# Kernel optimization log

Hardware: AMD Instinct MI355X
Metric: run time of the kernel (lower is better)

## Reference

```python
import jax, jax.numpy as jnp
import numpy as np

N_NODES = 50000
N_EDGES = 800000
NEG_SLOPE = 0.2


def gat_conv(x, src, dst, W, att_src, att_dst, bias, heads, out_ch, concat):
    """PyG-style GATConv (eval mode, self-loops already included in src/dst)."""
    N = x.shape[0]
    h = (x @ W).reshape(N, heads, out_ch)                      # [N,H,C]
    a_src = (h * att_src).sum(-1)                              # [N,H]
    a_dst = (h * att_dst).sum(-1)                              # [N,H]
    alpha = jax.nn.leaky_relu(a_src[src] + a_dst[dst], NEG_SLOPE)  # [E,H]
    # numerically stable segment softmax over incoming edges of each dst node
    amax = jax.ops.segment_max(alpha, dst, num_segments=N)     # [N,H]
    amax = jax.lax.stop_gradient(jnp.where(jnp.isfinite(amax), amax, 0.0))
    ex = jnp.exp(alpha - amax[dst])                            # [E,H]
    denom = jax.ops.segment_sum(ex, dst, num_segments=N)       # [N,H]
    coef = ex / (denom[dst] + 1e-16)                           # [E,H]
    msg = h[src] * coef[..., None]                             # [E,H,C]
    out = jax.ops.segment_sum(msg, dst, num_segments=N)        # [N,H,C]
    out = out.reshape(N, heads * out_ch) if concat else out.mean(axis=1)
    return out + bias


def setup_inputs() -> dict:
    key = jax.random.key(0)
    ks = jax.random.split(key, 12)
    x = jax.random.normal(ks[0], (N_NODES, 2), dtype=jnp.float32)
    edge_index = jax.random.randint(ks[1], (2, N_EDGES), 0, N_NODES, dtype=jnp.int64)
    # layer1: 2 -> 32, heads=4, concat
    W1 = jax.random.normal(ks[2], (2, 4 * 32), dtype=jnp.float32) * 0.5
    att_src1 = jax.random.normal(ks[3], (1, 4, 32), dtype=jnp.float32) * 0.1
    att_dst1 = jax.random.normal(ks[4], (1, 4, 32), dtype=jnp.float32) * 0.1
    b1 = jax.random.normal(ks[5], (128,), dtype=jnp.float32) * 0.01
    # layer2: 128 -> 128, heads=1, concat=False
    W2 = jax.random.normal(ks[6], (128, 128), dtype=jnp.float32) * (1.0 / np.sqrt(128.0))
    att_src2 = jax.random.normal(ks[7], (1, 1, 128), dtype=jnp.float32) * 0.1
    att_dst2 = jax.random.normal(ks[8], (1, 1, 128), dtype=jnp.float32) * 0.1
    b2 = jax.random.normal(ks[9], (128,), dtype=jnp.float32) * 0.01
    return {"x": x, "edge_index": edge_index, "W1": W1, "att_src1": att_src1,
            "att_dst1": att_dst1, "b1": b1, "W2": W2, "att_src2": att_src2,
            "att_dst2": att_dst2, "b2": b2}


def reference(x, edge_index, W1, att_src1, att_dst1, b1, W2, att_src2, att_dst2, b2):
    N = x.shape[0]
    loops = jnp.arange(N, dtype=edge_index.dtype)
    src = jnp.concatenate([edge_index[0], loops])  # PyG add_self_loops=True
    dst = jnp.concatenate([edge_index[1], loops])
    h = gat_conv(x, src, dst, W1, att_src1, att_dst1, b1, 4, 32, True)
    h = jax.nn.relu(h)
    h = gat_conv(h, src, dst, W2, att_src2, att_dst2, b2, 1, 128, False)
    # global_mean_pool with a single graph (batch all zeros) then squeeze(0)
    return h.mean(axis=0)  # [128]
```

## Files before the change

kernel.cpp:

```cpp
#include <hip/hip_runtime.h>

#define NN 50000
#define NE 800000
#define ET (NE + NN)
#define EPW 4096
#define NWGP ((ET + EPW - 1) / EPW)
#define NB 196
#define BCAP 6144

typedef unsigned short u16;
typedef unsigned int u32;
typedef unsigned char u8;

__device__ __forceinline__ float lrelu(float a) { return a > 0.f ? a : 0.2f * a; }

__global__ __launch_bounds__(256) void k_init(
        u32* __restrict__ bcur, u32* __restrict__ bcur2,
        u32* __restrict__ ovf, u32* __restrict__ ovf2,
        float* __restrict__ z, int* __restrict__ off, int* __restrict__ off_s,
        const float* __restrict__ W1, const float* __restrict__ as1,
        const float* __restrict__ ad1, const float* __restrict__ W2,
        const float* __restrict__ as2, const float* __restrict__ ad2,
        float* __restrict__ AD, float* __restrict__ vs, float* __restrict__ vd) {
    int i = threadIdx.x;
    bcur[i] = 0; bcur2[i] = 0;
    if (i == 0) { *ovf = 0; *ovf2 = 0; off[NN] = ET; off_s[NN] = ET; }
    if (i < 128) {
        z[i] = 0.f;
        float a = 0.f, d = 0.f;
        for (int c = 0; c < 128; ++c) {
            float wv = W2[i * 128 + c];
            a = fmaf(wv, as2[c], a);
            d = fmaf(wv, ad2[c], d);
        }
        vs[i] = a; vd[i] = d;
    }
    if (i >= 128 && i < 144) {
        int q = i - 128, isD = q >> 3, j = (q >> 2) & 1, hd = q & 3;
        const float* att = isD ? ad1 : as1;
        float acc = 0.f;
        for (int ch = 0; ch < 32; ++ch)
            acc = fmaf(W1[j * 128 + hd * 32 + ch], att[hd * 32 + ch], acc);
        AD[isD * 8 + j * 4 + hd] = acc;
    }
}

__global__ __launch_bounds__(256) void k_part(
        const int* __restrict__ ei,
        u32* __restrict__ bcur, u32* __restrict__ bcur2,
        u32* __restrict__ stg, u32* __restrict__ stg_s,
        u32* __restrict__ stg2, u32* __restrict__ stg2s,
        u32* __restrict__ ovf, u32* __restrict__ ovf2) {
    __shared__ u32 lcnt[256], sc[256], lbase[256], gbase[256];
    __shared__ u32 lpair[EPW];
    __shared__ u8  lbkt[EPW];
    int t = threadIdx.x;
    int e0 = blockIdx.x * EPW;

    u32 pr[16]; bool vd_[16]; u16 rk[16]; u8 bk[16];
#pragma unroll
    for (int j = 0; j < 16; ++j) {
        int e = e0 + j * 256 + t;
        vd_[j] = (e < ET);
        if (vd_[j]) {
            int s, d;
            if (e < NE) { s = ei[e]; d = ei[NE + e]; } else { s = d = e - NE; }
            pr[j] = ((u32)d << 16) | (u32)s;
        }
    }
    lcnt[t] = 0;
    __syncthreads();
#pragma unroll
    for (int j = 0; j < 16; ++j) if (vd_[j]) {
        int b = pr[j] >> 24;
        bk[j] = (u8)b;
        rk[j] = (u16)atomicAdd(&lcnt[b], 1u);
    }
    __syncthreads();
    u32 v = lcnt[t];
    sc[t] = v;
    __syncthreads();
#pragma unroll
    for (int st = 1; st < 256; st <<= 1) {
        u32 u = (t >= st) ? sc[t - st] : 0;
        __syncthreads();
        sc[t] += u;
        __syncthreads();
    }
    lbase[t] = sc[t] - v;
    gbase[t] = atomicAdd(&bcur[t], v);
    __syncthreads();
#pragma unroll
    for (int j = 0; j < 16; ++j) if (vd_[j]) {
        u32 idx = lbase[bk[j]] + rk[j];
        lpair[idx] = pr[j];
        lbkt[idx]  = bk[j];
    }
    __syncthreads();
    int nloc = lbase[255] + lcnt[255];
    for (int i = t; i < nloc; i += 256) {
        u32 b = lbkt[i];
        u32 g = gbase[b] + (i - lbase[b]);
        u32 p = lpair[i];
        if (g < BCAP) stg[(size_t)b * BCAP + g] = p;
        else { u32 o = atomicAdd(ovf, 1u); if (o < 4096) stg2[o] = p; }
    }
    __syncthreads();
    lcnt[t] = 0;
    __syncthreads();
#pragma unroll
    for (int j = 0; j < 16; ++j) if (vd_[j]) {
        int b = (pr[j] & 0xFFFFu) >> 8;
        bk[j] = (u8)b;
        rk[j] = (u16)atomicAdd(&lcnt[b], 1u);
    }
    __syncthreads();
    v = lcnt[t];
    sc[t] = v;
    __syncthreads();
#pragma unroll
    for (int st = 1; st < 256; st <<= 1) {
        u32 u = (t >= st) ? sc[t - st] : 0;
        __syncthreads();
        sc[t] += u;
        __syncthreads();
    }
    lbase[t] = sc[t] - v;
    gbase[t] = atomicAdd(&bcur2[t], v);
    __syncthreads();
#pragma unroll
    for (int j = 0; j < 16; ++j) if (vd_[j]) {
        u32 p2 = (pr[j] << 16) | (pr[j] >> 16);
        u32 idx = lbase[bk[j]] + rk[j];
        lpair[idx] = p2;
        lbkt[idx]  = bk[j];
    }
    __syncthreads();
    nloc = lbase[255] + lcnt[255];
    for (int i = t; i < nloc; i += 256) {
        u32 b = lbkt[i];
        u32 g = gbase[b] + (i - lbase[b]);
        u32 p = lpair[i];
        if (g < BCAP) stg_s[(size_t)b * BCAP + g] = p;
        else { u32 o = atomicAdd(ovf2, 1u); if (o < 4096) stg2s[o] = p; }
    }
}

__global__ __launch_bounds__(256) void k_place2(
        const u32* __restrict__ bcurA, const u32* __restrict__ bcurB,
        const u32* __restrict__ stgA, const u32* __restrict__ stgB,
        const u32* __restrict__ stg2A, const u32* __restrict__ stg2B,
        const u32* __restrict__ ovfA, const u32* __restrict__ ovfB,
        int* __restrict__ offA, int* __restrict__ offB,
        u16* __restrict__ outA, u16* __restrict__ outB) {
    __shared__ u32 sh[256], hist[256], sc[256], lcur[256];
    __shared__ u16 lcsr[BCAP];
    int blk = blockIdx.x, t = threadIdx.x;
    bool isB = (blk >= NB);
    int b = isB ? blk - NB : blk;
    const u32* bcur = isB ? bcurB : bcurA;
    const u32* stg  = isB ? stgB  : stgA;
    const u32* stg2 = isB ? stg2B : stg2A;
    const u32* ovf  = isB ? ovfB  : ovfA;
    int* off   = isB ? offB : offA;
    u16* out16 = isB ? outB : outA;

    u32 vv = (t < NB) ? bcur[t] : 0;
    sh[t] = vv;
    hist[t] = 0;
    __syncthreads();
#pragma unroll
    for (int s = 1; s < 256; s <<= 1) {
        u32 u = (t >= s) ? sh[t - s] : 0;
        __syncthreads();
        sh[t] += u;
        __syncthreads();
    }
    int S0 = (int)(sh[b] - bcur[b]);
    u32 cnt = bcur[b];
    u32 cmain = min(cnt, (u32)BCAP);

    for (u32 i = t; i < cmain; i += 256)
        atomicAdd(&hist[(stg[(size_t)b * BCAP + i] >> 16) & 255u], 1u);
    if (cnt > cmain) {
        u32 no = min(*ovf, 4096u);
        for (u32 i = t; i < no; i += 256) {
            u32 p = stg2[i];
            if ((p >> 24) == (u32)b) atomicAdd(&hist[(p >> 16) & 255u], 1u);
        }
    }
    __syncthreads();
    u32 v = hist[t];
    sc[t] = v;
    __syncthreads();
#pragma unroll
    for (int s = 1; s < 256; s <<= 1) {
        u32 u = (t >= s) ? sc[t - s] : 0;
        __syncthreads();
        sc[t] += u;
        __syncthreads();
    }
    u32 lexcl = sc[t] - v;
    int n = (b << 8) + t;
    if (n < NN) off[n] = S0 + (int)lexcl;
    lcur[t] = lexcl;
    __syncthreads();
    bool direct = (cnt > (u32)BCAP);
    for (u32 i = t; i < cmain; i += 256) {
        u32 p = stg[(size_t)b * BCAP + i];
        u32 r = atomicAdd(&lcur[(p >> 16) & 255u], 1u);
        if (direct) out16[S0 + r] = (u16)(p & 0xFFFFu);
        else        lcsr[r] = (u16)(p & 0xFFFFu);
    }
    if (cnt > cmain) {
        u32 no = min(*ovf, 4096u);
        for (u32 i = t; i < no; i += 256) {
            u32 p = stg2[i];
            if ((p >> 24) == (u32)b) {
                u32 r = atomicAdd(&lcur[(p >> 16) & 255u], 1u);
                if (direct) out16[S0 + r] = (u16)(p & 0xFFFFu);
                else        lcsr[r] = (u16)(p & 0xFFFFu);
            }
        }
    }
    __syncthreads();
    if (!direct)
        for (u32 i = t; i < cnt; i += 256) out16[S0 + i] = lcsr[i];
}

__global__ __launch_bounds__(128) void k_agg1x(
        const int* __restrict__ off, const u16* __restrict__ csr,
        const float* __restrict__ x, const float* __restrict__ AD,
        const float* __restrict__ W1, const float* __restrict__ b1,
        const float* __restrict__ vs, const float* __restrict__ vd,
        float* __restrict__ x2, float* __restrict__ asrc2,
        float* __restrict__ adst2) {
    __shared__ float sW1[256], sb1[128], svs[128], svd[128];
    int t = threadIdx.x;
    if (t < 128) {
        sW1[t] = W1[t]; sW1[128 + t] = W1[128 + t];
        sb1[t] = b1[t]; svs[t] = vs[t]; svd[t] = vd[t];
    }
    __syncthreads();
    int g = t >> 4, li = t & 15;
    int n = blockIdx.x * 8 + g;
    if (n >= NN) return;
    int e0 = off[n], deg = off[n + 1] - e0;
    float2 xd = *(const float2*)(x + 2 * n);
    float A0[4], A1[4], adn[4];
#pragma unroll
    for (int h = 0; h < 4; ++h) {
        A0[h] = AD[h]; A1[h] = AD[4 + h];
        adn[h] = fmaf(AD[8 + h], xd.x, AD[12 + h] * xd.y);
    }

    float den[4] = {0.f, 0.f, 0.f, 0.f};
    float S0[4] = {0.f, 0.f, 0.f, 0.f};
    float S1[4] = {0.f, 0.f, 0.f, 0.f};
    for (int e = li; e < deg; e += 16) {
        int s = csr[e0 + e];
        float2 xv = *(const float2*)(x + 2 * s);
#pragma unroll
        for (int h = 0; h < 4; ++h) {
            float al = lrelu(fmaf(A0[h], xv.x, A1[h] * xv.y) + adn[h]);
            float ex = __expf(fminf(al, 80.f));
            den[h] += ex;
            S0[h] = fmaf(ex, xv.x, S0[h]);
            S1[h] = fmaf(ex, xv.y, S1[h]);
        }
    }
#pragma unroll
    for (int m = 8; m >= 1; m >>= 1) {
#pragma unroll
        for (int h = 0; h < 4; ++h) {
            den[h] += __shfl_xor(den[h], m);
            S0[h]  += __shfl_xor(S0[h], m);
            S1[h]  += __shfl_xor(S1[h], m);
        }
    }
    float inv[4];
#pragma unroll
    for (int h = 0; h < 4; ++h) inv[h] = 1.f / (den[h] + 1e-16f);

    int hd = li >> 2;
    float ov[8];
    float ps = 0.f, pd = 0.f;
#pragma unroll
    for (int k = 0; k < 8; ++k) {
        int c = li * 8 + k;
        float o = (S0[hd] * sW1[c] + S1[hd] * sW1[128 + c]) * inv[hd];
        float v = fmaxf(o + sb1[c], 0.f);
        ov[k] = v;
        ps = fmaf(v, svs[c], ps);
        pd = fmaf(v, svd[c], pd);
    }
    *(float4*)(x2 + (size_t)n * 128 + li * 8) =
        make_float4(ov[0], ov[1], ov[2], ov[3]);
    *(float4*)(x2 + (size_t)n * 128 + li * 8 + 4) =
        make_float4(ov[4], ov[5], ov[6], ov[7]);
#pragma unroll
    for (int m = 8; m >= 1; m >>= 1) {
        ps += __shfl_xor(ps, m);
        pd += __shfl_xor(pd, m);
    }
    if (li == 0) { asrc2[n] = ps; adst2[n] = pd; }
}

__global__ __launch_bounds__(128) void k_den(
        const int* __restrict__ off, const u16* __restrict__ csr,
        const float* __restrict__ asrc2, const float* __restrict__ adst2,
        float2* __restrict__ dd) {
    int t = threadIdx.x;
    int g = t >> 4, li = t & 15;
    int n = blockIdx.x * 8 + g;
    if (n >= NN) return;
    int e0 = off[n], deg = off[n + 1] - e0;
    float adn = adst2[n];
    float den = 0.f;
    for (int e = li; e < deg; e += 16)
        den += __expf(fminf(lrelu(asrc2[csr[e0 + e]] + adn), 80.f));
#pragma unroll
    for (int m = 8; m >= 1; m >>= 1) den += __shfl_xor(den, m);
    if (li == 0) dd[n] = make_float2(adn, 1.f / (den + 1e-16f));
}

__global__ __launch_bounds__(128) void k_wgath(
        const int* __restrict__ off_s, const u16* __restrict__ csc,
        const float* __restrict__ asrc2, const float2* __restrict__ dd,
        float* __restrict__ w) {
    int t = threadIdx.x;
    int g = t >> 4, li = t & 15;
    int n = blockIdx.x * 8 + g;
    if (n >= NN) return;
    int e0 = off_s[n], deg = off_s[n + 1] - e0;
    float as = asrc2[n];
    float acc = 0.f;
    for (int e = li; e < deg; e += 16) {
        float2 di = dd[csc[e0 + e]];
        acc = fmaf(__expf(fminf(lrelu(as + di.x), 80.f)), di.y, acc);
    }
#pragma unroll
    for (int m = 8; m >= 1; m >>= 1) acc += __shfl_xor(acc, m);
    if (li == 0) w[n] = acc;
}

__global__ __launch_bounds__(256) void k_wsum(const float* __restrict__ w,
                                              const float* __restrict__ x2,
                                              float* __restrict__ z) {
    __shared__ float red[256];
    int t = threadIdx.x, c = t & 127, rp = t >> 7;
    float acc = 0.f;
    for (int n = blockIdx.x * 2 + rp; n < NN; n += 2048)
        acc = fmaf(w[n], x2[(size_t)n * 128 + c], acc);
    red[t] = acc;
    __syncthreads();
    if (t < 128) atomicAdd(z + t, red[t] + red[t + 128]);
}

__global__ __launch_bounds__(128) void k_out(const float* __restrict__ z,
                                             const float* __restrict__ W2,
                                             const float* __restrict__ b2,
                                             float* __restrict__ out) {
    int c = threadIdx.x;
    float acc = 0.f;
    for (int k = 0; k < 128; ++k)
        acc = fmaf(z[k], W2[k * 128 + c], acc);
    out[c] = b2[c] + acc * (1.0f / NN);
}

extern "C" void kernel_launch(void* const* d_in, const int* in_sizes, int n_in,
                              void* d_out, int out_size, void* d_ws, size_t ws_size,
                              hipStream_t stream) {
    const float* x   = (const float*)d_in[0];
    const int*   ei  = (const int*)d_in[1];
    const float* W1  = (const float*)d_in[2];
    const float* as1 = (const float*)d_in[3];
    const float* ad1 = (const float*)d_in[4];
    const float* b1  = (const float*)d_in[5];
    const float* W2  = (const float*)d_in[6];
    const float* as2 = (const float*)d_in[7];
    const float* ad2 = (const float*)d_in[8];
    const float* b2  = (const float*)d_in[9];
    float* out = (float*)d_out;

    char* ws     = (char*)d_ws;
    float* x2    = (float*)ws;
    u32*  stg    = (u32*)x2;
    u32*  stg_s  = stg + (size_t)NB * BCAP;
    float* w     = x2 + (size_t)NN * 128;
    float* asrc2 = w + NN;
    float* adst2 = asrc2 + NN;
    float2* dd   = (float2*)(adst2 + NN);
    int* off     = (int*)(dd + NN);
    int* off_s   = off + NN + 1;
    u32* bcur    = (u32*)(off_s + NN + 1);
    u32* bcur2   = bcur + 256;
    u32* ovf     = bcur2 + 256;
    u32* ovf2    = ovf + 4;
    u32* stg2    = ovf2 + 4;
    u32* stg2s   = stg2 + 4096;
    u16* csr16   = (u16*)(stg2s + 4096);
    u16* csc16   = csr16 + ET;
    float* AD    = (float*)(csc16 + ET);
    float* vs    = AD + 16;
    float* vd    = vs + 128;
    float* z     = vd + 128;

    k_init<<<1, 256, 0, stream>>>(bcur, bcur2, ovf, ovf2, z, off, off_s,
                                  W1, as1, ad1, W2, as2, ad2, AD, vs, vd);
    k_part<<<NWGP, 256, 0, stream>>>(ei, bcur, bcur2, stg, stg_s,
                                     stg2, stg2s, ovf, ovf2);
    k_place2<<<2 * NB, 256, 0, stream>>>(bcur, bcur2, stg, stg_s,
                                         stg2, stg2s, ovf, ovf2,
                                         off, off_s, csr16, csc16);
    k_agg1x<<<(NN + 7) / 8, 128, 0, stream>>>(off, csr16, x, AD, W1, b1,
                                              vs, vd, x2, asrc2, adst2);
    k_den<<<(NN + 7) / 8, 128, 0, stream>>>(off, csr16, asrc2, adst2, dd);
    k_wgath<<<(NN + 7) / 8, 128, 0, stream>>>(off_s, csc16, asrc2, dd, w);
    k_wsum<<<1024, 256, 0, stream>>>(w, x2, z);
    k_out<<<1, 128, 0, stream>>>(z, W2, b2, out);
}
```

Before: 123.5 us.

## Use wave-shuffle scans, halve partition tile, fuse final reduction with output

Replaces the shared-memory Hillis-Steele prefix scans (many __syncthreads per scan) with a 64-lane shuffle scan plus a 4-wave combine in the partition and placement kernels. Halves edges per partition workgroup so more workgroups run and fewer registers are needed per thread. Fuses the final weighted-sum and output matmul kernels using a last-block-done counter, removing one launch. The trade-offs are more global atomics on the bucket counters from the extra workgroups and a grid-wide completion counter that relies on correct fencing.

```diff
diff --git a/kernel.cpp b/kernel.cpp
--- a/kernel.cpp
+++ b/kernel.cpp
@@ -3,10 +3,12 @@
 #define NN 50000
 #define NE 800000
 #define ET (NE + NN)
-#define EPW 4096
+#define EPW 2048
+#define EPT (EPW / 256)
 #define NWGP ((ET + EPW - 1) / EPW)
 #define NB 196
 #define BCAP 6144
+#define WSB 1024
 
 typedef unsigned short u16;
 typedef unsigned int u32;
@@ -14,9 +16,18 @@
 
 __device__ __forceinline__ float lrelu(float a) { return a > 0.f ? a : 0.2f * a; }
 
+__device__ __forceinline__ u32 wave_iscan(u32 v, int lane) {
+#pragma unroll
+    for (int d = 1; d < 64; d <<= 1) {
+        u32 u = __shfl_up(v, d);
+        if (lane >= d) v += u;
+    }
+    return v;
+}
+
 __global__ __launch_bounds__(256) void k_init(
         u32* __restrict__ bcur, u32* __restrict__ bcur2,
-        u32* __restrict__ ovf, u32* __restrict__ ovf2,
+        u32* __restrict__ ovf, u32* __restrict__ ovf2, u32* __restrict__ cnt,
         float* __restrict__ z, int* __restrict__ off, int* __restrict__ off_s,
         const float* __restrict__ W1, const float* __restrict__ as1,
         const float* __restrict__ ad1, const float* __restrict__ W2,
@@ -24,7 +35,7 @@
         float* __restrict__ AD, float* __restrict__ vs, float* __restrict__ vd) {
     int i = threadIdx.x;
     bcur[i] = 0; bcur2[i] = 0;
-    if (i == 0) { *ovf = 0; *ovf2 = 0; off[NN] = ET; off_s[NN] = ET; }
+    if (i == 0) { *ovf = 0; *ovf2 = 0; *cnt = 0; off[NN] = ET; off_s[NN] = ET; }
     if (i < 128) {
         z[i] = 0.f;
         float a = 0.f, d = 0.f;
@@ -51,15 +62,16 @@
         u32* __restrict__ stg, u32* __restrict__ stg_s,
         u32* __restrict__ stg2, u32* __restrict__ stg2s,
         u32* __restrict__ ovf, u32* __restrict__ ovf2) {
-    __shared__ u32 lcnt[256], sc[256], lbase[256], gbase[256];
+    __shared__ u32 lcnt[256], lbase[256], gbase[256], wsums[4];
     __shared__ u32 lpair[EPW];
     __shared__ u8  lbkt[EPW];
     int t = threadIdx.x;
+    int lane = t & 63, wid = t >> 6;
     int e0 = blockIdx.x * EPW;
 
-    u32 pr[16]; bool vd_[16]; u16 rk[16]; u8 bk[16];
-#pragma unroll
-    for (int j = 0; j < 16; ++j) {
+    u32 pr[EPT]; bool vd_[EPT]; u16 rk[EPT]; u8 bk[EPT];
+#pragma unroll
+    for (int j = 0; j < EPT; ++j) {
         int e = e0 + j * 256 + t;
         vd_[j] = (e < ET);
         if (vd_[j]) {
@@ -71,27 +83,24 @@
     lcnt[t] = 0;
     __syncthreads();
 #pragma unroll
-    for (int j = 0; j < 16; ++j) if (vd_[j]) {
+    for (int j = 0; j < EPT; ++j) if (vd_[j]) {
         int b = pr[j] >> 24;
         bk[j] = (u8)b;
         rk[j] = (u16)atomicAdd(&lcnt[b], 1u);
     }
     __syncthreads();
     u32 v = lcnt[t];
-    sc[t] = v;
-    __syncthreads();
-#pragma unroll
-    for (int st = 1; st < 256; st <<= 1) {
-        u32 u = (t >= st) ? sc[t - st] : 0;
-        __syncthreads();
-        sc[t] += u;
-        __syncthreads();
-    }
-    lbase[t] = sc[t] - v;
+    u32 inc = wave_iscan(v, lane);
+    if (lane == 63) wsums[wid] = inc;
+    __syncthreads();
+    u32 base = 0;
+#pragma unroll
+    for (int k = 0; k < 4; ++k) base += (k < wid) ? wsums[k] : 0;
+    lbase[t] = base + inc - v;
     gbase[t] = atomicAdd(&bcur[t], v);
     __syncthreads();
 #pragma unroll
-    for (int j = 0; j < 16; ++j) if (vd_[j]) {
+    for (int j = 0; j < EPT; ++j) if (vd_[j]) {
         u32 idx = lbase[bk[j]] + rk[j];
         lpair[idx] = pr[j];
         lbkt[idx]  = bk[j];
@@ -109,27 +118,24 @@
     lcnt[t] = 0;
     __syncthreads();
 #pragma unroll
-    for (int j = 0; j < 16; ++j) if (vd_[j]) {
+    for (int j = 0; j < EPT; ++j) if (vd_[j]) {
         int b = (pr[j] & 0xFFFFu) >> 8;
         bk[j] = (u8)b;
         rk[j] = (u16)atomicAdd(&lcnt[b], 1u);
     }
     __syncthreads();
     v = lcnt[t];
-    sc[t] = v;
-    __syncthreads();
-#pragma unroll
-    for (int st = 1; st < 256; st <<= 1) {
-        u32 u = (t >= st) ? sc[t - st] : 0;
-        __syncthreads();
-        sc[t] += u;
-        __syncthreads();
-    }
-    lbase[t] = sc[t] - v;
+    inc = wave_iscan(v, lane);
+    if (lane == 63) wsums[wid] = inc;
+    __syncthreads();
+    base = 0;
+#pragma unroll
+    for (int k = 0; k < 4; ++k) base += (k < wid) ? wsums[k] : 0;
+    lbase[t] = base + inc - v;
     gbase[t] = atomicAdd(&bcur2[t], v);
     __syncthreads();
 #pragma unroll
-    for (int j = 0; j < 16; ++j) if (vd_[j]) {
+    for (int j = 0; j < EPT; ++j) if (vd_[j]) {
         u32 p2 = (pr[j] << 16) | (pr[j] >> 16);
         u32 idx = lbase[bk[j]] + rk[j];
         lpair[idx] = p2;
@@ -153,9 +159,10 @@
         const u32* __restrict__ ovfA, const u32* __restrict__ ovfB,
         int* __restrict__ offA, int* __restrict__ offB,
         u16* __restrict__ outA, u16* __restrict__ outB) {
-    __shared__ u32 sh[256], hist[256], sc[256], lcur[256];
+    __shared__ u32 sh[256], hist[256], lcur[256], wsums[4];
     __shared__ u16 lcsr[BCAP];
     int blk = blockIdx.x, t = threadIdx.x;
+    int lane = t & 63, wid = t >> 6;
     bool isB = (blk >= NB);
     int b = isB ? blk - NB : blk;
     const u32* bcur = isB ? bcurB : bcurA;
@@ -166,17 +173,16 @@
     u16* out16 = isB ? outB : outA;
 
     u32 vv = (t < NB) ? bcur[t] : 0;
-    sh[t] = vv;
+    u32 inc = wave_iscan(vv, lane);
+    if (lane == 63) wsums[wid] = inc;
     hist[t] = 0;
     __syncthreads();
-#pragma unroll
-    for (int s = 1; s < 256; s <<= 1) {
-        u32 u = (t >= s) ? sh[t - s] : 0;
-        __syncthreads();
-        sh[t] += u;
-        __syncthreads();
-    }
-    int S0 = (int)(sh[b] - bcur[b]);
+    u32 base = 0;
+#pragma unroll
+    for (int k = 0; k < 4; ++k) base += (k < wid) ? wsums[k] : 0;
+    sh[t] = base + inc - vv;
+    __syncthreads();
+    int S0 = (int)sh[b];
     u32 cnt = bcur[b];
     u32 cmain = min(cnt, (u32)BCAP);
 
@@ -191,16 +197,13 @@
     }
     __syncthreads();
     u32 v = hist[t];
-    sc[t] = v;
-    __syncthreads();
-#pragma unroll
-    for (int s = 1; s < 256; s <<= 1) {
-        u32 u = (t >= s) ? sc[t - s] : 0;
-        __syncthreads();
-        sc[t] += u;
-        __syncthreads();
-    }
-    u32 lexcl = sc[t] - v;
+    u32 inc2 = wave_iscan(v, lane);
+    if (lane == 63) wsums[wid] = inc2;
+    __syncthreads();
+    u32 base2 = 0;
+#pragma unroll
+    for (int k = 0; k < 4; ++k) base2 += (k < wid) ? wsums[k] : 0;
+    u32 lexcl = base2 + inc2 - v;
     int n = (b << 8) + t;
     if (n < NN) off[n] = S0 + (int)lexcl;
     lcur[t] = lexcl;
@@ -344,28 +347,35 @@
     if (li == 0) w[n] = acc;
 }
 
-__global__ __launch_bounds__(256) void k_wsum(const float* __restrict__ w,
-                                              const float* __restrict__ x2,
-                                              float* __restrict__ z) {
+__global__ __launch_bounds__(256) void k_wsum_out(
+        const float* __restrict__ w, const float* __restrict__ x2,
+        float* __restrict__ z, const float* __restrict__ W2,
+        const float* __restrict__ b2, float* __restrict__ out,
+        u32* __restrict__ cnt) {
     __shared__ float red[256];
+    __shared__ float zs[128];
+    __shared__ int lastf;
     int t = threadIdx.x, c = t & 127, rp = t >> 7;
     float acc = 0.f;
-    for (int n = blockIdx.x * 2 + rp; n < NN; n += 2048)
+    for (int n = blockIdx.x * 2 + rp; n < NN; n += WSB * 2)
         acc = fmaf(w[n], x2[(size_t)n * 128 + c], acc);
     red[t] = acc;
     __syncthreads();
     if (t < 128) atomicAdd(z + t, red[t] + red[t + 128]);
-}
-
-__global__ __launch_bounds__(128) void k_out(const float* __restrict__ z,
-                                             const float* __restrict__ W2,
-                                             const float* __restrict__ b2,
-                                             float* __restrict__ out) {
-    int c = threadIdx.x;
-    float acc = 0.f;
-    for (int k = 0; k < 128; ++k)
-        acc = fmaf(z[k], W2[k * 128 + c], acc);
-    out[c] = b2[c] + acc * (1.0f / NN);
+    __threadfence();
+    __syncthreads();
+    if (t == 0) lastf = (atomicAdd(cnt, 1u) == WSB - 1) ? 1 : 0;
+    __syncthreads();
+    if (lastf) {
+        if (t < 128) zs[t] = atomicAdd(z + t, 0.f);
+        __syncthreads();
+        if (t < 128) {
+            float a2 = 0.f;
+            for (int k = 0; k < 128; ++k)
+                a2 = fmaf(zs[k], W2[k * 128 + t], a2);
+            out[t] = b2[t] + a2 * (1.0f / NN);
+        }
+    }
 }
 
 extern "C" void kernel_launch(void* const* d_in, const int* in_sizes, int n_in,
@@ -397,7 +407,8 @@
     u32* bcur2   = bcur + 256;
     u32* ovf     = bcur2 + 256;
     u32* ovf2    = ovf + 4;
-    u32* stg2    = ovf2 + 4;
+    u32* cnt     = ovf2 + 4;
+    u32* stg2    = cnt + 4;
     u32* stg2s   = stg2 + 4096;
     u16* csr16   = (u16*)(stg2s + 4096);
     u16* csc16   = csr16 + ET;
@@ -406,7 +417,7 @@
     float* vd    = vs + 128;
     float* z     = vd + 128;
 
-    k_init<<<1, 256, 0, stream>>>(bcur, bcur2, ovf, ovf2, z, off, off_s,
+    k_init<<<1, 256, 0, stream>>>(bcur, bcur2, ovf, ovf2, cnt, z, off, off_s,
                                   W1, as1, ad1, W2, as2, ad2, AD, vs, vd);
     k_part<<<NWGP, 256, 0, stream>>>(ei, bcur, bcur2, stg, stg_s,
                                      stg2, stg2s, ovf, ovf2);
@@ -417,6 +428,5 @@
                                               vs, vd, x2, asrc2, adst2);
     k_den<<<(NN + 7) / 8, 128, 0, stream>>>(off, csr16, asrc2, adst2, dd);
     k_wgath<<<(NN + 7) / 8, 128, 0, stream>>>(off_s, csc16, asrc2, dd, w);
-    k_wsum<<<1024, 256, 0, stream>>>(w, x2, z);
-    k_out<<<1, 128, 0, stream>>>(z, W2, b2, out);
-}
+    k_wsum_out<<<WSB, 256, 0, stream>>>(w, x2, z, W2, b2, out, cnt);
+}
```

New measurement: 159.0 us. 28.7% more time.
